# Kernel tuning notes

Measured on AMD Instinct MI355X. Metric: run time of the kernel, lower is better.

The kernel has to match this reference:

```python
import jax, jax.numpy as jnp
import numpy as np

MAX_DUR = 4      # durations sampled in [0, 4], so padded output len = Tmax * MAX_DUR
PAD_VALUE = 0.0  # LengthRegulator pad_value


def setup_inputs() -> dict:
    key = jax.random.key(0)
    k1, k2 = jax.random.split(key)
    B, T, D = 16, 1024, 384
    xs = jax.random.normal(k1, (B, T, D), dtype=jnp.float32)
    ds = jax.random.randint(k2, (B, T), 0, MAX_DUR + 1, dtype=jnp.int32)
    return {"xs": xs, "ds": ds}


def reference(xs, ds):
    """Duration-based repeat-interleave + pad (FastSpeech length regulator).

    Equivalent math to: [repeat_interleave(x, d, dim=0) for x, d in zip(xs, ds)]
    followed by pad_list(..., pad_value), except the padded length is the static
    capacity T*MAX_DUR instead of the data-dependent batch max (extra columns
    are pure pad_value). For output frame t of sample b, the source token is
    the i with cumsum(ds)[b, i-1] <= t < cumsum(ds)[b, i].
    """
    B, T, D = xs.shape
    out_len = T * MAX_DUR  # static output capacity

    cs = jnp.cumsum(ds, axis=1)                      # (B, T) cumulative durations
    t = jnp.arange(out_len, dtype=cs.dtype)          # (out_len,)
    # source index per output frame: count of cumsums <= t
    idx = jax.vmap(lambda c: jnp.searchsorted(c, t, side="right"))(cs)  # (B, out_len)
    valid = t[None, :] < cs[:, -1:]                  # (B, out_len) within total length
    idx = jnp.minimum(idx, T - 1)

    gathered = jnp.take_along_axis(xs, idx[:, :, None], axis=1)  # (B, out_len, D)
    return jnp.where(valid[:, :, None], gathered, jnp.asarray(PAD_VALUE, xs.dtype))
```

## Files before the change

### kernel.cpp

```cpp
#include <hip/hip_runtime.h>
#include <hip/hip_bf16.h>

#define B_SZ 16
#define T_SZ 1024
#define D_SZ 384
#define MAX_DUR 4
#define OUT_LEN (T_SZ * MAX_DUR)
#define C4 (D_SZ / 4)
#define N4 (B_SZ * OUT_LEN * C4)

__global__ __launch_bounds__(256) void prep_kernel(const int* __restrict__ ds,
                                                   int* __restrict__ srcArr) {
    __shared__ int sums[256];
    __shared__ int cs[T_SZ + 1];
    const int b   = blockIdx.x;
    const int tid = threadIdx.x;

    int4 v = ((const int4*)(ds + b * T_SZ))[tid];
    const int s0 = v.x;
    const int s1 = s0 + v.y;
    const int s2 = s1 + v.z;
    const int s3 = s2 + v.w;

    sums[tid] = s3;
    __syncthreads();

    int val = s3;
    for (int off = 1; off < 256; off <<= 1) {
        int other = (tid >= off) ? sums[tid - off] : 0;
        __syncthreads();
        val += other;
        sums[tid] = val;
        __syncthreads();
    }

    const int excl = val - s3;
    if (tid == 0) cs[0] = 0;
    cs[4 * tid + 1] = excl + s0;
    cs[4 * tid + 2] = excl + s1;
    cs[4 * tid + 3] = excl + s2;
    cs[4 * tid + 4] = excl + s3;
    __syncthreads();

    const int total = cs[T_SZ];
    int* row = srcArr + b * OUT_LEN;

    #pragma unroll
    for (int j = 0; j < 4; ++j) {
        const int i   = 4 * tid + j;
        const int st  = cs[i];
        const int en  = cs[i + 1];
        const int src = (b * T_SZ + i) * C4;
        for (int t = st; t < en; ++t) row[t] = src;
    }
    for (int t = total + tid; t < OUT_LEN; t += 256) row[t] = -1;
}

__global__ __launch_bounds__(256) void regulate_kernel(const float4* __restrict__ xs4,
                                                       const int* __restrict__ srcArr,
                                                       float4* __restrict__ out4) {
    const int g0 = blockIdx.x * 1024 + threadIdx.x;
    #pragma unroll
    for (int k = 0; k < 4; ++k) {
        const int g   = g0 + k * 256;
        const int f   = g / 96;
        const int col = g - f * 96;
        const int s   = srcArr[f];
        float4 v = make_float4(0.0f, 0.0f, 0.0f, 0.0f);
        if (s >= 0) v = xs4[s + col];
        out4[g] = v;
    }
}

extern "C" void kernel_launch(void* const* d_in, const int* in_sizes, int n_in,
                              void* d_out, int out_size, void* d_ws, size_t ws_size,
                              hipStream_t stream) {
    const float4* xs4 = (const float4*)d_in[0];
    const int*    ds  = (const int*)d_in[1];
    float4*       out4 = (float4*)d_out;
    int*          srcArr = (int*)d_ws;

    prep_kernel<<<B_SZ, 256, 0, stream>>>(ds, srcArr);

    regulate_kernel<<<N4 / 1024, 256, 0, stream>>>(xs4, srcArr, out4);
}
```

Baseline: 129.1 us.

## Fuse prefix-sum prep into gather kernel with per-block shared-memory frame map

Merges the two kernels into one. Each block redoes the per-sample cumulative sum of durations and builds a 4096-entry frame-to-source map in shared memory, then writes a contiguous slice of that sample's output, 16 float4 per thread. This removes the second launch, the dependency between the two kernels, and the global round trip of the index array. The cost is that the scan and map construction are repeated by all 96 blocks of each sample, and the 16 KB of shared memory per block may limit occupancy.

```diff
diff --git a/kernel.cpp b/kernel.cpp
--- a/kernel.cpp
+++ b/kernel.cpp
@@ -7,14 +7,20 @@
 #define MAX_DUR 4
 #define OUT_LEN (T_SZ * MAX_DUR)
 #define C4 (D_SZ / 4)
-#define N4 (B_SZ * OUT_LEN * C4)
+#define PER_SAMPLE_F4 (OUT_LEN * C4)
+#define BLOCKS_PER_SAMPLE 96
+#define ITERS 16
 
-__global__ __launch_bounds__(256) void prep_kernel(const int* __restrict__ ds,
-                                                   int* __restrict__ srcArr) {
+__global__ __launch_bounds__(256) void lenreg_fused(const float4* __restrict__ xs4,
+                                                    const int* __restrict__ ds,
+                                                    float4* __restrict__ out4) {
     __shared__ int sums[256];
-    __shared__ int cs[T_SZ + 1];
-    const int b   = blockIdx.x;
+    __shared__ int map[OUT_LEN];
+    __shared__ int s_total;
+
     const int tid = threadIdx.x;
+    const int b   = blockIdx.x / BLOCKS_PER_SAMPLE;
+    const int blk = blockIdx.x - b * BLOCKS_PER_SAMPLE;
 
     int4 v = ((const int4*)(ds + b * T_SZ))[tid];
     const int s0 = v.x;
@@ -33,42 +39,37 @@
         sums[tid] = val;
         __syncthreads();
     }
+    const int excl = val - s3;
+    if (tid == 255) s_total = val;
 
-    const int excl = val - s3;
-    if (tid == 0) cs[0] = 0;
-    cs[4 * tid + 1] = excl + s0;
-    cs[4 * tid + 2] = excl + s1;
-    cs[4 * tid + 3] = excl + s2;
-    cs[4 * tid + 4] = excl + s3;
+    const int srcBase = (b * T_SZ + 4 * tid) * C4;
+    {
+        int st = excl, en = excl + s0;
+        for (int t = st; t < en; ++t) map[t] = srcBase;
+        st = en; en = excl + s1;
+        for (int t = st; t < en; ++t) map[t] = srcBase + C4;
+        st = en; en = excl + s2;
+        for (int t = st; t < en; ++t) map[t] = srcBase + 2 * C4;
+        st = en; en = excl + s3;
+        for (int t = st; t < en; ++t) map[t] = srcBase + 3 * C4;
+    }
     __syncthreads();
 
-    const int total = cs[T_SZ];
-    int* row = srcArr + b * OUT_LEN;
+    const int total = s_total;
+    for (int t = total + tid; t < OUT_LEN; t += 256) map[t] = -1;
+    __syncthreads();
 
+    const int base = blk * (ITERS * 256);
+    float4* outp = out4 + (size_t)b * PER_SAMPLE_F4;
     #pragma unroll
-    for (int j = 0; j < 4; ++j) {
-        const int i   = 4 * tid + j;
-        const int st  = cs[i];
-        const int en  = cs[i + 1];
-        const int src = (b * T_SZ + i) * C4;
-        for (int t = st; t < en; ++t) row[t] = src;
-    }
-    for (int t = total + tid; t < OUT_LEN; t += 256) row[t] = -1;
-}
-
-__global__ __launch_bounds__(256) void regulate_kernel(const float4* __restrict__ xs4,
-                                                       const int* __restrict__ srcArr,
-                                                       float4* __restrict__ out4) {
-    const int g0 = blockIdx.x * 1024 + threadIdx.x;
-    #pragma unroll
-    for (int k = 0; k < 4; ++k) {
-        const int g   = g0 + k * 256;
-        const int f   = g / 96;
-        const int col = g - f * 96;
-        const int s   = srcArr[f];
-        float4 v = make_float4(0.0f, 0.0f, 0.0f, 0.0f);
-        if (s >= 0) v = xs4[s + col];
-        out4[g] = v;
+    for (int k = 0; k < ITERS; ++k) {
+        const int g   = base + k * 256 + tid;
+        const int f   = g / C4;
+        const int col = g - f * C4;
+        const int s   = map[f];
+        float4 o = make_float4(0.0f, 0.0f, 0.0f, 0.0f);
+        if (s >= 0) o = xs4[s + col];
+        outp[g] = o;
     }
 }
 
@@ -78,9 +79,6 @@
     const float4* xs4 = (const float4*)d_in[0];
     const int*    ds  = (const int*)d_in[1];
     float4*       out4 = (float4*)d_out;
-    int*          srcArr = (int*)d_ws;
 
-    prep_kernel<<<B_SZ, 256, 0, stream>>>(ds, srcArr);
-
-    regulate_kernel<<<N4 / 1024, 256, 0, stream>>>(xs4, srcArr, out4);
+    lenreg_fused<<<B_SZ * BLOCKS_PER_SAMPLE, 256, 0, stream>>>(xs4, ds, out4);
 }
```

Result: no change. 128.0 us (-0.8%).
